# Optimization experiments

Measured on AMD Instinct MI355X. Metric: run time of the kernel, lower is better.

Reference implementation:

```python
import jax, jax.numpy as jnp
import numpy as np

OUT_LEN = 25  # fixed self.out_length
H1, H2, D_IN, D_OUT = 9, 32, 5, 3


def _rnn_last(x_tbd, Wih, Whh, b):
    """Elman tanh RNN, time-major input [T,B,D]; returns final hidden [B,H]."""
    B = x_tbd.shape[1]
    h0 = jnp.zeros((B, Wih.shape[0]), x_tbd.dtype)
    def step(h, x_t):
        h = jnp.tanh(x_t @ Wih.T + h @ Whh.T + b)
        return h, None
    h_last, _ = jax.lax.scan(step, h0, x_tbd)
    return h_last


def _rnn_all(x_tbd, Wih, Whh, b):
    """Elman tanh RNN, time-major input [T,B,D]; returns all hiddens [T,B,H]."""
    B = x_tbd.shape[1]
    h0 = jnp.zeros((B, Wih.shape[0]), x_tbd.dtype)
    def step(h, x_t):
        h = jnp.tanh(x_t @ Wih.T + h @ Whh.T + b)
        return h, h
    _, hs = jax.lax.scan(step, h0, x_tbd)
    return hs


def setup_inputs() -> dict:
    key = jax.random.key(0)
    ks = jax.random.split(key, 16)
    B, T = 4096, 2048
    s1 = 1.0 / np.sqrt(H1)
    s2 = 1.0 / np.sqrt(H2)
    u = lambda k, shp, s: jax.random.uniform(k, shp, jnp.float32, -s, s)
    return {
        "x": jax.random.uniform(ks[0], (B, T, D_IN), jnp.float32),
        # rnn_1 forward direction
        "w_ih_f": u(ks[1], (H1, D_IN), s1), "w_hh_f": u(ks[2], (H1, H1), s1),
        "b_ih_f": u(ks[3], (H1,), s1),     "b_hh_f": u(ks[4], (H1,), s1),
        # rnn_1 backward direction
        "w_ih_b": u(ks[5], (H1, D_IN), s1), "w_hh_b": u(ks[6], (H1, H1), s1),
        "b_ih_b": u(ks[7], (H1,), s1),      "b_hh_b": u(ks[8], (H1,), s1),
        # rnn_2 (input 2*H1=18, hidden 32)
        "w_ih2": u(ks[9], (H2, 2 * H1), s2), "w_hh2": u(ks[10], (H2, H2), s2),
        "b_ih2": u(ks[11], (H2,), s2),       "b_hh2": u(ks[12], (H2,), s2),
        # output linear 32 -> 3
        "w_out": u(ks[13], (D_OUT, H2), s2), "b_out": u(ks[14], (D_OUT,), s2),
    }


def reference(x, w_ih_f, w_hh_f, b_ih_f, b_hh_f,
              w_ih_b, w_hh_b, b_ih_b, b_hh_b,
              w_ih2, w_hh2, b_ih2, b_hh2, w_out, b_out):
    B = x.shape[0]
    xt = jnp.swapaxes(x, 0, 1)  # [T,B,5]
    h_f = _rnn_last(xt, w_ih_f, w_hh_f, b_ih_f + b_hh_f)          # [B,9]
    h_b = _rnn_last(xt[::-1], w_ih_b, w_hh_b, b_ih_b + b_hh_b)    # [B,9]
    y = jnp.concatenate([h_f, h_b], axis=1)                       # [B,18]
    # u: zeros over OUT_LEN steps with y at t=0 (time-major)
    u = jnp.zeros((OUT_LEN, B, 2 * H1), x.dtype).at[0].set(y)
    ys = _rnn_all(u, w_ih2, w_hh2, b_ih2 + b_hh2)                 # [25,B,32]
    ys = jnp.swapaxes(ys, 0, 1)                                   # [B,25,32]
    out = jnp.einsum('bth,oh->bto', ys, w_out) + b_out            # [B,25,3]
    return out
```

## Files before the change

### kernel.cpp

```cpp
#include <hip/hip_runtime.h>

#define RNN_T 2048
#define RNN_B 4096
#define BLK 16
#define NBLK (RNN_T / BLK)
#define CHF (BLK * 5)
#define WVF (4 * CHF)
#define BLF (16 * CHF)

__device__ __forceinline__ float tanh_pre(float zs) {
    float e = __builtin_amdgcn_exp2f(zs);
    float r = __builtin_amdgcn_rcpf(e + 1.0f);
    return fmaf(-2.0f, r, 1.0f);
}

__device__ __forceinline__ void async4(const float* src, float* dst) {
    __builtin_amdgcn_global_load_lds(
        (const __attribute__((address_space(1))) void*)src,
        (__attribute__((address_space(3))) void*)dst, 4, 0, 0);
}

__device__ __forceinline__ void fill_wave(float* dstWave, const float* (&src)[5],
                                          int adv) {
#pragma unroll
    for (int j = 0; j < 5; ++j) {
        async4(src[j], dstWave + j * 64);
        src[j] += adv;
    }
}

__device__ __forceinline__ void stepr(float& h, float xn, const float (&W)[16],
                                      float bb, bool own) {
    float a0 = fmaf(h, W[0], bb);
    float a1 = 0.0f, a2 = 0.0f;
    asm ("s_nop 1\n\t"
         "v_fmac_f32_dpp %0, %3, %4  row_ror:1  row_mask:0xf bank_mask:0xf\n\t"
         "v_fmac_f32_dpp %1, %3, %5  row_ror:2  row_mask:0xf bank_mask:0xf\n\t"
         "v_fmac_f32_dpp %2, %3, %6  row_ror:3  row_mask:0xf bank_mask:0xf\n\t"
         "v_fmac_f32_dpp %0, %3, %7  row_ror:4  row_mask:0xf bank_mask:0xf\n\t"
         "v_fmac_f32_dpp %1, %3, %8  row_ror:5  row_mask:0xf bank_mask:0xf\n\t"
         "v_fmac_f32_dpp %2, %3, %9  row_ror:6  row_mask:0xf bank_mask:0xf\n\t"
         "v_fmac_f32_dpp %0, %3, %10 row_ror:7  row_mask:0xf bank_mask:0xf\n\t"
         "v_fmac_f32_dpp %1, %3, %11 row_ror:8  row_mask:0xf bank_mask:0xf\n\t"
         "v_fmac_f32_dpp %2, %3, %12 row_ror:9  row_mask:0xf bank_mask:0xf\n\t"
         "v_fmac_f32_dpp %0, %3, %13 row_ror:10 row_mask:0xf bank_mask:0xf\n\t"
         "v_fmac_f32_dpp %1, %3, %14 row_ror:11 row_mask:0xf bank_mask:0xf\n\t"
         "v_fmac_f32_dpp %2, %3, %15 row_ror:12 row_mask:0xf bank_mask:0xf\n\t"
         "v_fmac_f32_dpp %0, %3, %16 row_ror:13 row_mask:0xf bank_mask:0xf\n\t"
         "v_fmac_f32_dpp %1, %3, %17 row_ror:14 row_mask:0xf bank_mask:0xf\n\t"
         "v_fmac_f32_dpp %2, %3, %18 row_ror:15 row_mask:0xf bank_mask:0xf"
         : "+v"(a0), "+v"(a1), "+v"(a2)
         : "v"(h), "v"(W[1]), "v"(W[2]), "v"(W[3]), "v"(W[4]), "v"(W[5]),
           "v"(W[6]), "v"(W[7]), "v"(W[8]), "v"(W[9]), "v"(W[10]), "v"(W[11]),
           "v"(W[12]), "v"(W[13]), "v"(W[14]), "v"(W[15]));
    const float z = (a0 + a1) + a2;
    const float t = tanh_pre(z);
    h = own ? t : xn;
}

template <bool FWD, bool FILL>
__device__ __forceinline__ void compute_block(const float* xc, const float* xnb,
        float& h, const float (&W)[16], float bb, bool own,
        float* fillDst, const float* (&src)[5], int adv) {
    float xn[16];
#pragma unroll
    for (int j = 0; j < 15; ++j) xn[j] = xc[FWD ? (j + 1) * 5 : (14 - j) * 5];
    xn[15] = xnb[FWD ? 0 : 75];
    if constexpr (FILL) fill_wave(fillDst, src, adv);
#pragma unroll
    for (int j = 0; j < 16; ++j) stepr(h, xn[j], W, bb, own);
}

template <bool FWD>
__device__ __forceinline__ float run_all(const float* xcA, const float* xcB,
        const float* xcC, float* wA, float* wB, float* wC,
        const float* (&src)[5], int adv,
        const float (&W)[16], float bb, bool own) {
    fill_wave(wA, src, adv);
    fill_wave(wB, src, adv);
    float h = own ? 0.0f : xcA[FWD ? 0 : 75];
#pragma unroll 1
    for (int it = 0; it < 42; ++it) {
        compute_block<FWD, true >(xcA, xcB, h, W, bb, own, wC, src, adv);
        compute_block<FWD, true >(xcB, xcC, h, W, bb, own, wA, src, adv);
        compute_block<FWD, true >(xcC, xcA, h, W, bb, own, wB, src, adv);
    }
    compute_block<FWD, false>(xcA, xcB, h, W, bb, own, wC, src, adv);
    compute_block<FWD, false>(xcB, xcB, h, W, bb, own, wC, src, adv);
    return h;
}

__global__ __launch_bounds__(256, 2) void rnn1_kernel(
    const float* __restrict__ x,
    const float* __restrict__ w_ih_f, const float* __restrict__ w_hh_f,
    const float* __restrict__ b_ih_f, const float* __restrict__ b_hh_f,
    const float* __restrict__ w_ih_b, const float* __restrict__ w_hh_b,
    const float* __restrict__ b_ih_b, const float* __restrict__ b_hh_b,
    float* __restrict__ y)
{
    __shared__ __align__(16) float sA[BLF], sB[BLF], sC[BLF];
    const float SC = 2.8853900817779268f;
    const int tid    = threadIdx.x;
    const int group  = tid >> 4;
    const int lane16 = tid & 15;
    const int waveId = tid >> 6;
    const int lane   = tid & 63;
    const int chain  = blockIdx.x * 16 + group;
    const int b      = chain & (RNN_B - 1);
    const int dir    = chain >> 12;

    const float* __restrict__ wih = dir ? w_ih_b : w_ih_f;
    const float* __restrict__ whh = dir ? w_hh_b : w_hh_f;
    const float* __restrict__ bih = dir ? b_ih_b : b_ih_f;
    const float* __restrict__ bhh = dir ? b_hh_b : b_hh_f;

    const int   li  = (lane16 < 9) ? lane16 : 0;
    const float msk = (lane16 < 9) ? SC : 0.0f;
    const bool  own = (lane16 < 9);
    float W[16];
#pragma unroll
    for (int r = 0; r < 16; ++r) {
        const int s = (lane16 - r) & 15;
        float w = 0.0f;
        if (s < 9)       w = whh[li * 9 + s];
        else if (s < 14) w = wih[li * 5 + (s - 9)];
        W[r] = w * msk;
    }
    const float bb = (bih[li] + bhh[li]) * msk;

    const float* src[5];
#pragma unroll
    for (int j = 0; j < 5; ++j) {
        const int idx = j * 64 + lane;
        const int gf  = idx / 80;
        const int p   = idx - gf * 80;
        const int bf  = (blockIdx.x * 16 + waveId * 4 + gf) & (RNN_B - 1);
        src[j] = x + (size_t)bf * (RNN_T * 5) + (dir ? (NBLK - 1) * CHF : 0) + p;
    }
    const int adv = dir ? -CHF : CHF;

    float* wA = sA + waveId * WVF;
    float* wB = sB + waveId * WVF;
    float* wC = sC + waveId * WVF;
    const int xoff = own ? 0 : ((lane16 < 14) ? (lane16 - 9) : 0);
    const float* xcA = sA + group * CHF + xoff;
    const float* xcB = sB + group * CHF + xoff;
    const float* xcC = sC + group * CHF + xoff;

    float h = dir ? run_all<false>(xcA, xcB, xcC, wA, wB, wC, src, adv, W, bb, own)
                  : run_all<true >(xcA, xcB, xcC, wA, wB, wC, src, adv, W, bb, own);

    if (lane16 < 9) y[b * 18 + dir * 9 + lane16] = h;
}

__global__ __launch_bounds__(256) void rnn2_kernel(
    const float* __restrict__ y,
    const float* __restrict__ w_ih2, const float* __restrict__ w_hh2,
    const float* __restrict__ b_ih2, const float* __restrict__ b_hh2,
    const float* __restrict__ w_out, const float* __restrict__ b_out,
    float* __restrict__ out)
{
    __shared__ float hist[8][25][32];
    const float SC = 2.8853900817779268f;
    const int bl = threadIdx.x >> 5;
    const int i  = threadIdx.x & 31;
    const int b  = blockIdx.x * 8 + bl;

    float wr[32];
#pragma unroll
    for (int k = 0; k < 32; ++k) wr[k] = w_hh2[i * 32 + k] * SC;
    const float bias = (b_ih2[i] + b_hh2[i]) * SC;

    const float* yb = y + b * 18;
    float z = bias;
#pragma unroll
    for (int k = 0; k < 18; ++k) z = fmaf(w_ih2[i * 18 + k] * SC, yb[k], z);
    hist[bl][0][i] = tanh_pre(z);
    __syncthreads();

    for (int t = 1; t < 25; ++t) {
        float zz = bias;
#pragma unroll
        for (int k = 0; k < 32; ++k) zz = fmaf(wr[k], hist[bl][t - 1][k], zz);
        hist[bl][t][i] = tanh_pre(zz);
        __syncthreads();
    }

    for (int e = threadIdx.x; e < 600; e += 256) {
        const int o  = e % 3;
        const int t  = (e / 3) % 25;
        const int b2 = e / 75;
        float acc = b_out[o];
#pragma unroll
        for (int k = 0; k < 32; ++k) acc = fmaf(w_out[o * 32 + k], hist[b2][t][k], acc);
        out[((size_t)(blockIdx.x * 8 + b2) * 25 + t) * 3 + o] = acc;
    }
}

extern "C" void kernel_launch(void* const* d_in, const int* in_sizes, int n_in,
                              void* d_out, int out_size, void* d_ws, size_t ws_size,
                              hipStream_t stream) {
    const float* x      = (const float*)d_in[0];
    const float* w_ih_f = (const float*)d_in[1];
    const float* w_hh_f = (const float*)d_in[2];
    const float* b_ih_f = (const float*)d_in[3];
    const float* b_hh_f = (const float*)d_in[4];
    const float* w_ih_b = (const float*)d_in[5];
    const float* w_hh_b = (const float*)d_in[6];
    const float* b_ih_b = (const float*)d_in[7];
    const float* b_hh_b = (const float*)d_in[8];
    const float* w_ih2  = (const float*)d_in[9];
    const float* w_hh2  = (const float*)d_in[10];
    const float* b_ih2  = (const float*)d_in[11];
    const float* b_hh2  = (const float*)d_in[12];
    const float* w_out  = (const float*)d_in[13];
    const float* b_out  = (const float*)d_in[14];

    float* y = (float*)d_ws;

    rnn1_kernel<<<dim3(512), dim3(256), 0, stream>>>(
        x, w_ih_f, w_hh_f, b_ih_f, b_hh_f,
        w_ih_b, w_hh_b, b_ih_b, b_hh_b, y);

    rnn2_kernel<<<dim3(RNN_B / 8), dim3(256), 0, stream>>>(
        y, w_ih2, w_hh2, b_ih2, b_hh2, w_out, b_out, (float*)d_out);
}
```

Measured before the change: 423.9 us.

## Pack two RNN chains per 16-lane row with interleaved DPP matvec

Reorganizes the first RNN kernel so each 16-lane DPP row serves two interleaved chains (8 lanes each) instead of one chain using 9 of 16 lanes. Each lane computes one hidden unit and lane 0 of each chain also computes unit 8 as a second state, so 32 chains fit per block and the grid halves to 256 blocks. The shared-memory staging doubles per wave and launch bounds drop to one block per SM. The aim is to use fewer wasted lanes per serial step, at the cost of two dependent tanh evaluations and more DPP instructions per step, plus lower occupancy for hiding latency.

```diff
diff --git a/kernel.cpp b/kernel.cpp
--- a/kernel.cpp
+++ b/kernel.cpp
@@ -5,8 +5,8 @@
 #define BLK 16
 #define NBLK (RNN_T / BLK)
 #define CHF (BLK * 5)
-#define WVF (4 * CHF)
-#define BLF (16 * CHF)
+#define WVF (8 * CHF)
+#define BLF (4 * WVF)
 
 __device__ __forceinline__ float tanh_pre(float zs) {
     float e = __builtin_amdgcn_exp2f(zs);
@@ -20,77 +20,115 @@
         (__attribute__((address_space(3))) void*)dst, 4, 0, 0);
 }
 
-__device__ __forceinline__ void fill_wave(float* dstWave, const float* (&src)[5],
+__device__ __forceinline__ void fill_wave(float* dstWave, const float* (&src)[10],
                                           int adv) {
 #pragma unroll
-    for (int j = 0; j < 5; ++j) {
+    for (int j = 0; j < 10; ++j) {
         async4(src[j], dstWave + j * 64);
         src[j] += adv;
     }
 }
 
-__device__ __forceinline__ void stepr(float& h, float xn, const float (&W)[16],
-                                      float bb, bool own) {
-    float a0 = fmaf(h, W[0], bb);
-    float a1 = 0.0f, a2 = 0.0f;
-    asm ("s_nop 1\n\t"
-         "v_fmac_f32_dpp %0, %3, %4  row_ror:1  row_mask:0xf bank_mask:0xf\n\t"
-         "v_fmac_f32_dpp %1, %3, %5  row_ror:2  row_mask:0xf bank_mask:0xf\n\t"
-         "v_fmac_f32_dpp %2, %3, %6  row_ror:3  row_mask:0xf bank_mask:0xf\n\t"
-         "v_fmac_f32_dpp %0, %3, %7  row_ror:4  row_mask:0xf bank_mask:0xf\n\t"
-         "v_fmac_f32_dpp %1, %3, %8  row_ror:5  row_mask:0xf bank_mask:0xf\n\t"
-         "v_fmac_f32_dpp %2, %3, %9  row_ror:6  row_mask:0xf bank_mask:0xf\n\t"
-         "v_fmac_f32_dpp %0, %3, %10 row_ror:7  row_mask:0xf bank_mask:0xf\n\t"
-         "v_fmac_f32_dpp %1, %3, %11 row_ror:8  row_mask:0xf bank_mask:0xf\n\t"
-         "v_fmac_f32_dpp %2, %3, %12 row_ror:9  row_mask:0xf bank_mask:0xf\n\t"
-         "v_fmac_f32_dpp %0, %3, %13 row_ror:10 row_mask:0xf bank_mask:0xf\n\t"
-         "v_fmac_f32_dpp %1, %3, %14 row_ror:11 row_mask:0xf bank_mask:0xf\n\t"
-         "v_fmac_f32_dpp %2, %3, %15 row_ror:12 row_mask:0xf bank_mask:0xf\n\t"
-         "v_fmac_f32_dpp %0, %3, %16 row_ror:13 row_mask:0xf bank_mask:0xf\n\t"
-         "v_fmac_f32_dpp %1, %3, %17 row_ror:14 row_mask:0xf bank_mask:0xf\n\t"
-         "v_fmac_f32_dpp %2, %3, %18 row_ror:15 row_mask:0xf bank_mask:0xf"
-         : "+v"(a0), "+v"(a1), "+v"(a2)
-         : "v"(h), "v"(W[1]), "v"(W[2]), "v"(W[3]), "v"(W[4]), "v"(W[5]),
-           "v"(W[6]), "v"(W[7]), "v"(W[8]), "v"(W[9]), "v"(W[10]), "v"(W[11]),
-           "v"(W[12]), "v"(W[13]), "v"(W[14]), "v"(W[15]));
-    const float z = (a0 + a1) + a2;
-    const float t = tanh_pre(z);
-    h = own ? t : xn;
+__device__ __forceinline__ void stepB(float& s0, float& s1, float xn,
+        const float (&Wa)[16], const float (&Wb)[16],
+        float bb0, float bb1, bool own8) {
+    float a0 = fmaf(s0, Wa[0], bb0);
+    float a1 = s1 * Wa[8];
+    float b0 = fmaf(s0, Wb[0], bb1);
+    float b1 = s1 * Wb[8];
+    asm("s_nop 1\n\t"
+        "v_fmac_f32_dpp %0, %2, %4  row_ror:2  row_mask:0xf bank_mask:0xf\n\t"
+        "v_fmac_f32_dpp %1, %3, %11 row_ror:2  row_mask:0xf bank_mask:0xf\n\t"
+        "v_fmac_f32_dpp %0, %2, %5  row_ror:4  row_mask:0xf bank_mask:0xf\n\t"
+        "v_fmac_f32_dpp %1, %3, %12 row_ror:4  row_mask:0xf bank_mask:0xf\n\t"
+        "v_fmac_f32_dpp %0, %2, %6  row_ror:6  row_mask:0xf bank_mask:0xf\n\t"
+        "v_fmac_f32_dpp %1, %3, %13 row_ror:6  row_mask:0xf bank_mask:0xf\n\t"
+        "v_fmac_f32_dpp %0, %2, %7  row_ror:8  row_mask:0xf bank_mask:0xf\n\t"
+        "v_fmac_f32_dpp %1, %3, %14 row_ror:8  row_mask:0xf bank_mask:0xf\n\t"
+        "v_fmac_f32_dpp %0, %2, %8  row_ror:10 row_mask:0xf bank_mask:0xf\n\t"
+        "v_fmac_f32_dpp %1, %3, %15 row_ror:10 row_mask:0xf bank_mask:0xf\n\t"
+        "v_fmac_f32_dpp %0, %2, %9  row_ror:12 row_mask:0xf bank_mask:0xf\n\t"
+        "v_fmac_f32_dpp %1, %3, %16 row_ror:12 row_mask:0xf bank_mask:0xf\n\t"
+        "v_fmac_f32_dpp %0, %2, %10 row_ror:14 row_mask:0xf bank_mask:0xf\n\t"
+        "v_fmac_f32_dpp %1, %3, %17 row_ror:14 row_mask:0xf bank_mask:0xf"
+        : "+v"(a0), "+v"(a1)
+        : "v"(s0), "v"(s1),
+          "v"(Wa[1]), "v"(Wa[2]), "v"(Wa[3]), "v"(Wa[4]), "v"(Wa[5]),
+          "v"(Wa[6]), "v"(Wa[7]),
+          "v"(Wa[9]), "v"(Wa[10]), "v"(Wa[11]), "v"(Wa[12]), "v"(Wa[13]),
+          "v"(Wa[14]), "v"(Wa[15]));
+    asm("s_nop 1\n\t"
+        "v_fmac_f32_dpp %0, %2, %4  row_ror:2  row_mask:0xf bank_mask:0xf\n\t"
+        "v_fmac_f32_dpp %1, %3, %11 row_ror:2  row_mask:0xf bank_mask:0xf\n\t"
+        "v_fmac_f32_dpp %0, %2, %5  row_ror:4  row_mask:0xf bank_mask:0xf\n\t"
+        "v_fmac_f32_dpp %1, %3, %12 row_ror:4  row_mask:0xf bank_mask:0xf\n\t"
+        "v_fmac_f32_dpp %0, %2, %6  row_ror:6  row_mask:0xf bank_mask:0xf\n\t"
+        "v_fmac_f32_dpp %1, %3, %13 row_ror:6  row_mask:0xf bank_mask:0xf\n\t"
+        "v_fmac_f32_dpp %0, %2, %7  row_ror:8  row_mask:0xf bank_mask:0xf\n\t"
+        "v_fmac_f32_dpp %1, %3, %14 row_ror:8  row_mask:0xf bank_mask:0xf\n\t"
+        "v_fmac_f32_dpp %0, %2, %8  row_ror:10 row_mask:0xf bank_mask:0xf\n\t"
+        "v_fmac_f32_dpp %1, %3, %15 row_ror:10 row_mask:0xf bank_mask:0xf\n\t"
+        "v_fmac_f32_dpp %0, %2, %9  row_ror:12 row_mask:0xf bank_mask:0xf\n\t"
+        "v_fmac_f32_dpp %1, %3, %16 row_ror:12 row_mask:0xf bank_mask:0xf\n\t"
+        "v_fmac_f32_dpp %0, %2, %10 row_ror:14 row_mask:0xf bank_mask:0xf\n\t"
+        "v_fmac_f32_dpp %1, %3, %17 row_ror:14 row_mask:0xf bank_mask:0xf"
+        : "+v"(b0), "+v"(b1)
+        : "v"(s0), "v"(s1),
+          "v"(Wb[1]), "v"(Wb[2]), "v"(Wb[3]), "v"(Wb[4]), "v"(Wb[5]),
+          "v"(Wb[6]), "v"(Wb[7]),
+          "v"(Wb[9]), "v"(Wb[10]), "v"(Wb[11]), "v"(Wb[12]), "v"(Wb[13]),
+          "v"(Wb[14]), "v"(Wb[15]));
+    const float z0 = a0 + a1;
+    const float z1 = b0 + b1;
+    const float t1 = tanh_pre(z1);
+    s0 = tanh_pre(z0);
+    s1 = own8 ? t1 : xn;
 }
 
 template <bool FWD, bool FILL>
 __device__ __forceinline__ void compute_block(const float* xc, const float* xnb,
-        float& h, const float (&W)[16], float bb, bool own,
-        float* fillDst, const float* (&src)[5], int adv) {
+        float& s0, float& s1, const float (&Wa)[16], const float (&Wb)[16],
+        float bb0, float bb1, bool own8,
+        float* fillDst, const float* (&src)[10], int adv) {
     float xn[16];
 #pragma unroll
     for (int j = 0; j < 15; ++j) xn[j] = xc[FWD ? (j + 1) * 5 : (14 - j) * 5];
     xn[15] = xnb[FWD ? 0 : 75];
     if constexpr (FILL) fill_wave(fillDst, src, adv);
 #pragma unroll
-    for (int j = 0; j < 16; ++j) stepr(h, xn[j], W, bb, own);
+    for (int j = 0; j < 16; ++j)
+        stepB(s0, s1, xn[j], Wa, Wb, bb0, bb1, own8);
 }
 
 template <bool FWD>
-__device__ __forceinline__ float run_all(const float* xcA, const float* xcB,
+__device__ __forceinline__ void run_all(const float* xcA, const float* xcB,
         const float* xcC, float* wA, float* wB, float* wC,
-        const float* (&src)[5], int adv,
-        const float (&W)[16], float bb, bool own) {
+        const float* (&src)[10], int adv,
+        const float (&Wa)[16], const float (&Wb)[16], float bb0, float bb1,
+        bool own8, float& s0, float& s1) {
     fill_wave(wA, src, adv);
     fill_wave(wB, src, adv);
-    float h = own ? 0.0f : xcA[FWD ? 0 : 75];
+    s0 = 0.0f;
+    const float pr = xcA[FWD ? 0 : 75];
+    s1 = own8 ? 0.0f : pr;
 #pragma unroll 1
     for (int it = 0; it < 42; ++it) {
-        compute_block<FWD, true >(xcA, xcB, h, W, bb, own, wC, src, adv);
-        compute_block<FWD, true >(xcB, xcC, h, W, bb, own, wA, src, adv);
-        compute_block<FWD, true >(xcC, xcA, h, W, bb, own, wB, src, adv);
-    }
-    compute_block<FWD, false>(xcA, xcB, h, W, bb, own, wC, src, adv);
-    compute_block<FWD, false>(xcB, xcB, h, W, bb, own, wC, src, adv);
-    return h;
-}
-
-__global__ __launch_bounds__(256, 2) void rnn1_kernel(
+        compute_block<FWD, true >(xcA, xcB, s0, s1, Wa, Wb, bb0, bb1, own8, wC, src, adv);
+        compute_block<FWD, true >(xcB, xcC, s0, s1, Wa, Wb, bb0, bb1, own8, wA, src, adv);
+        compute_block<FWD, true >(xcC, xcA, s0, s1, Wa, Wb, bb0, bb1, own8, wB, src, adv);
+    }
+    compute_block<FWD, false>(xcA, xcB, s0, s1, Wa, Wb, bb0, bb1, own8, wC, src, adv);
+    compute_block<FWD, false>(xcB, xcB, s0, s1, Wa, Wb, bb0, bb1, own8, wC, src, adv);
+}
+
+__device__ __forceinline__ float wfull(const float* wih, const float* whh,
+                                       int row, int c) {
+    if (c < 9)  return whh[row * 9 + c];
+    if (c < 14) return wih[row * 5 + (c - 9)];
+    return 0.0f;
+}
+
+__global__ __launch_bounds__(256, 1) void rnn1_kernel(
     const float* __restrict__ x,
     const float* __restrict__ w_ih_f, const float* __restrict__ w_hh_f,
     const float* __restrict__ b_ih_f, const float* __restrict__ b_hh_f,
@@ -101,11 +139,14 @@
     __shared__ __align__(16) float sA[BLF], sB[BLF], sC[BLF];
     const float SC = 2.8853900817779268f;
     const int tid    = threadIdx.x;
-    const int group  = tid >> 4;
-    const int lane16 = tid & 15;
     const int waveId = tid >> 6;
     const int lane   = tid & 63;
-    const int chain  = blockIdx.x * 16 + group;
+    const int l16    = lane & 15;
+    const int row16  = lane >> 4;
+    const int par    = l16 & 1;
+    const int c0     = l16 >> 1;
+    const int chainL = row16 * 2 + par;
+    const int chain  = blockIdx.x * 32 + waveId * 8 + chainL;
     const int b      = chain & (RNN_B - 1);
     const int dir    = chain >> 12;
 
@@ -114,27 +155,26 @@
     const float* __restrict__ bih = dir ? b_ih_b : b_ih_f;
     const float* __restrict__ bhh = dir ? b_hh_b : b_hh_f;
 
-    const int   li  = (lane16 < 9) ? lane16 : 0;
-    const float msk = (lane16 < 9) ? SC : 0.0f;
-    const bool  own = (lane16 < 9);
-    float W[16];
-#pragma unroll
-    for (int r = 0; r < 16; ++r) {
-        const int s = (lane16 - r) & 15;
-        float w = 0.0f;
-        if (s < 9)       w = whh[li * 9 + s];
-        else if (s < 14) w = wih[li * 5 + (s - 9)];
-        W[r] = w * msk;
-    }
-    const float bb = (bih[li] + bhh[li]) * msk;
-
-    const float* src[5];
-#pragma unroll
-    for (int j = 0; j < 5; ++j) {
+    const bool own8 = (c0 == 0);
+    float Wa[16], Wb[16];
+#pragma unroll
+    for (int j = 0; j < 2; ++j)
+#pragma unroll
+        for (int r = 0; r < 8; ++r) {
+            const int c = ((c0 - r) & 7) + 8 * j;
+            Wa[j * 8 + r] = wfull(wih, whh, c0, c) * SC;
+            Wb[j * 8 + r] = own8 ? (wfull(wih, whh, 8, c) * SC) : 0.0f;
+        }
+    const float bb0 = (bih[c0] + bhh[c0]) * SC;
+    const float bb1 = own8 ? ((bih[8] + bhh[8]) * SC) : 0.0f;
+
+    const float* src[10];
+#pragma unroll
+    for (int j = 0; j < 10; ++j) {
         const int idx = j * 64 + lane;
         const int gf  = idx / 80;
         const int p   = idx - gf * 80;
-        const int bf  = (blockIdx.x * 16 + waveId * 4 + gf) & (RNN_B - 1);
+        const int bf  = (blockIdx.x * 32 + waveId * 8 + gf) & (RNN_B - 1);
         src[j] = x + (size_t)bf * (RNN_T * 5) + (dir ? (NBLK - 1) * CHF : 0) + p;
     }
     const int adv = dir ? -CHF : CHF;
@@ -142,15 +182,19 @@
     float* wA = sA + waveId * WVF;
     float* wB = sB + waveId * WVF;
     float* wC = sC + waveId * WVF;
-    const int xoff = own ? 0 : ((lane16 < 14) ? (lane16 - 9) : 0);
-    const float* xcA = sA + group * CHF + xoff;
-    const float* xcB = sB + group * CHF + xoff;
-    const float* xcC = sC + group * CHF + xoff;
-
-    float h = dir ? run_all<false>(xcA, xcB, xcC, wA, wB, wC, src, adv, W, bb, own)
-                  : run_all<true >(xcA, xcB, xcC, wA, wB, wC, src, adv, W, bb, own);
-
-    if (lane16 < 9) y[b * 18 + dir * 9 + lane16] = h;
+    const int cx = (c0 >= 1 && c0 <= 5) ? (c0 - 1) : 0;
+    const float* xcA = sA + waveId * WVF + chainL * CHF + cx;
+    const float* xcB = sB + waveId * WVF + chainL * CHF + cx;
+    const float* xcC = sC + waveId * WVF + chainL * CHF + cx;
+
+    float s0, s1;
+    if (dir) run_all<false>(xcA, xcB, xcC, wA, wB, wC, src, adv,
+                            Wa, Wb, bb0, bb1, own8, s0, s1);
+    else     run_all<true >(xcA, xcB, xcC, wA, wB, wC, src, adv,
+                            Wa, Wb, bb0, bb1, own8, s0, s1);
+
+    y[b * 18 + dir * 9 + c0] = s0;
+    if (l16 < 2) y[b * 18 + dir * 9 + 8] = s1;
 }
 
 __global__ __launch_bounds__(256) void rnn2_kernel(
@@ -218,7 +262,7 @@
 
     float* y = (float*)d_ws;
 
-    rnn1_kernel<<<dim3(512), dim3(256), 0, stream>>>(
+    rnn1_kernel<<<dim3(256), dim3(256), 0, stream>>>(
         x, w_ih_f, w_hh_f, b_ih_f, b_hh_f,
         w_ih_b, w_hh_b, b_ih_b, b_hh_b, y);
 
```

New measurement: 454.8 us. 7.3% more time.
